# Optimization experiments

Measured on AMD Instinct MI355X. Metric: run time of the kernel, lower is better.

The kernel has to match this reference:

```python
import jax, jax.numpy as jnp
import numpy as np

N = 50000   # nodes
E = 800000  # edges (avg degree 16)
G = 64      # graphs in batch
DIN = 96
DH = 96
DOUT = 10
MD = 30


def setup_inputs() -> dict:
    key = jax.random.key(0)
    ks = jax.random.split(key, 13)
    s = lambda d: 1.0 / np.sqrt(d)
    return {
        "x": jax.random.normal(ks[0], (N, DIN), jnp.float32),
        "edge_index": jax.random.randint(ks[1], (2, E), 0, N, dtype=jnp.int64),
        "edge_attr": jax.random.uniform(ks[2], (E,), jnp.float32),
        "batch": jnp.sort(jax.random.randint(ks[3], (N,), 0, G, dtype=jnp.int64)),
        "metadata": jax.random.normal(ks[4], (G, MD), jnp.float32),
        "W1": jax.random.normal(ks[5], (DIN, DH), jnp.float32) * s(DIN),
        "b1": jnp.zeros((DH,), jnp.float32),
        "W2": jax.random.normal(ks[6], (DH, DH), jnp.float32) * s(DH),
        "b2": jnp.zeros((DH,), jnp.float32),
        "Wm": jax.random.normal(ks[7], (MD, DH), jnp.float32) * s(MD),
        "bm": jnp.zeros((DH,), jnp.float32),
        "Wf": jax.random.normal(ks[8], (2 * DH, DOUT), jnp.float32) * s(2 * DH),
        "bf": jnp.zeros((DOUT,), jnp.float32),
    }


def gcn_conv(x, src, dst, w, W, b):
    """PyG GCNConv with edge weights and self-loops (fill value 1.0)."""
    h = x @ W  # [N, dh]
    deg = jax.ops.segment_sum(w, dst, num_segments=N) + 1.0  # self-loop weight 1
    dinv = jax.lax.rsqrt(deg)
    norm = dinv[src] * w * dinv[dst]  # [E]
    msg = h[src] * norm[:, None]      # gather + weight: [E, dh]
    agg = jax.ops.segment_sum(msg, dst, num_segments=N)
    agg = agg + h * (dinv * dinv)[:, None]  # self-loop contribution
    return agg + b


def reference(x, edge_index, edge_attr, batch, metadata,
              W1, b1, W2, b2, Wm, bm, Wf, bf):
    src, dst = edge_index[0], edge_index[1]
    h = jax.nn.relu(gcn_conv(x, src, dst, edge_attr, W1, b1))
    h = jax.nn.relu(gcn_conv(h, src, dst, edge_attr, W2, b2))
    # global mean pool over graphs
    sums = jax.ops.segment_sum(h, batch, num_segments=G)
    cnts = jax.ops.segment_sum(jnp.ones((N,), h.dtype), batch, num_segments=G)
    pooled = sums / jnp.maximum(cnts, 1.0)[:, None]  # [G, dh]
    # first node index of each graph (batch is sorted), then idx % metadata rows
    first_idx = jax.ops.segment_min(jnp.arange(N), batch, num_segments=G)
    md = metadata[first_idx % metadata.shape[0]]  # [G, 30]
    md_h = jax.nn.relu(md @ Wm + bm)  # dropout = identity in eval
    z = jnp.concatenate([pooled, md_h], axis=1)  # [G, 2*dh]
    return z @ Wf + bf
```

## Files before the change

### kernel.cpp

```cpp
#include <hip/hip_runtime.h>
#include <hip/hip_bf16.h>
#include <cstdint>

typedef unsigned long long ull;
typedef unsigned int uint;

#define FIXS 4194304.0f
#define CAPMAX 48

__device__ __forceinline__ void fma4(float4& a, float s, const float4& v) {
    a.x += s * v.x; a.y += s * v.y; a.z += s * v.z; a.w += s * v.w;
}
__device__ __forceinline__ float dinv_of(ull q) {
    return rsqrtf((float)(unsigned)(q & 0xffffffffULL) * (1.0f / FIXS) + 1.0f);
}
__device__ __forceinline__ uint bf16r(float f) {
    uint u = __float_as_uint(f);
    u += 0x7FFF + ((u >> 16) & 1);
    return u >> 16;
}
__device__ __forceinline__ uint pkbf(float a, float b) { return bf16r(a) | (bf16r(b) << 16); }
__device__ __forceinline__ float blo(uint u) { return __uint_as_float(u << 16); }
__device__ __forceinline__ float bhi(uint u) { return __uint_as_float(u & 0xffff0000u); }


__device__ __forceinline__ void edge_body(int e, const int* __restrict__ ei, const float* __restrict__ w,
                                          ull* __restrict__ packed, int2* __restrict__ ell, int CAP, int E) {
    if (e >= E) return;
    int s = ei[e], d = ei[E + e];
    float wv = w[e];
    ull inc = (1ULL << 32) | (ull)(unsigned)(wv * FIXS + 0.5f);
    ull old = atomicAdd(&packed[d], inc);
    int pos = (int)(old >> 32);
    if (pos < CAP) ell[(size_t)d * CAP + pos] = make_int2(s, __float_as_int(wv));
}

__device__ __forceinline__ void gemm_body(float* Ws, int bb, const float* __restrict__ X,
                                          const float* __restrict__ W, uint* __restrict__ Hb, int N) {
    int t = threadIdx.x;
    {
        const float4* Wg = (const float4*)W;
        float4* Wl = (float4*)Ws;
        for (int i = t; i < 2304; i += 256) Wl[i] = Wg[i];
    }
    int lane = t & 63, wv = t >> 6;
    int cb = wv * 6;
    int row0 = bb * 128;
    int rA = row0 + lane, rB = row0 + 64 + lane;
    bool vA = rA < N, vB = rB < N;
    const float* xA = X + (size_t)(vA ? rA : 0) * 96;
    const float* xB = X + (size_t)(vB ? rB : 0) * 96;
    __syncthreads();
    float4 aA[6] = {}, aB[6] = {};
    const float4* W4 = (const float4*)Ws;
    for (int k0 = 0; k0 < 96; k0 += 4) {
        float4 xa = *(const float4*)(xA + k0);
        float4 xb = *(const float4*)(xB + k0);
#pragma unroll
        for (int kk = 0; kk < 4; kk++) {
            float sa = (kk == 0) ? xa.x : (kk == 1) ? xa.y : (kk == 2) ? xa.z : xa.w;
            float sb = (kk == 0) ? xb.x : (kk == 1) ? xb.y : (kk == 2) ? xb.z : xb.w;
#pragma unroll
            for (int c = 0; c < 6; c++) {
                float4 wv4 = W4[(k0 + kk) * 24 + cb + c];
                fma4(aA[c], sa, wv4);
                fma4(aB[c], sb, wv4);
            }
        }
    }
    if (vA) {
        uint4* o = (uint4*)(Hb + (size_t)rA * 48 + wv * 12);
#pragma unroll
        for (int c = 0; c < 3; c++)
            o[c] = make_uint4(pkbf(aA[2*c].x, aA[2*c].y), pkbf(aA[2*c].z, aA[2*c].w),
                              pkbf(aA[2*c+1].x, aA[2*c+1].y), pkbf(aA[2*c+1].z, aA[2*c+1].w));
    }
    if (vB) {
        uint4* o = (uint4*)(Hb + (size_t)rB * 48 + wv * 12);
#pragma unroll
        for (int c = 0; c < 3; c++)
            o[c] = make_uint4(pkbf(aB[2*c].x, aB[2*c].y), pkbf(aB[2*c].z, aB[2*c].w),
                              pkbf(aB[2*c+1].x, aB[2*c+1].y), pkbf(aB[2*c+1].z, aB[2*c+1].w));
    }
}

__device__ __forceinline__ void pool_meta_body(int bb, const int* __restrict__ batch,
                                               int* __restrict__ cnts, int* __restrict__ firstmax, int N) {
    int n = bb * 256 + threadIdx.x;
    int lane = threadIdx.x & 63;
    bool valid = n < N;
    int g = valid ? batch[n] : -1;
    int gp = __shfl_up(g, 1);
    bool leader = valid && (lane == 0 || gp != g);
    ull lm = __ballot(leader);
    if (leader) {
        ull higher = (lane == 63) ? 0ULL : (lm >> (lane + 1));
        int run;
        if (higher) {
            run = __ffsll((long long)higher);
        } else {
            int waveBase = n - lane;
            int validLanes = min(64, N - waveBase);
            run = validLanes - lane;
        }
        atomicAdd(&cnts[g], run);
        atomicMax(&firstmax[g], N - n);
    }
}

__global__ __launch_bounds__(256) void k_phase1(const float* __restrict__ X, const float* __restrict__ W1,
                                                uint* __restrict__ H1b,
                                                const int* __restrict__ ei, const float* __restrict__ w,
                                                ull* __restrict__ packed, int2* __restrict__ ell, int CAP, int E,
                                                const int* __restrict__ batch, int* __restrict__ cnts,
                                                int* __restrict__ firstmax, int N, int GB, int PB) {
    __shared__ __align__(16) float Ws[96 * 96];
    int b = blockIdx.x;
    if (b < GB) {
        gemm_body(Ws, b, X, W1, H1b, N);
    } else if (b < GB + PB) {
        pool_meta_body(b - GB, batch, cnts, firstmax, N);
    } else {
        edge_body((b - GB - PB) * 256 + threadIdx.x, ei, w, packed, ell, CAP, E);
    }
}

__device__ __forceinline__ float4 gather24(const int2* nbr, int j, int c, int n, float dn, float d2,
                                           const uint* __restrict__ hb, const float* __restrict__ bias) {
    int jo = 2 * j;
    uint2 su = *(const uint2*)(hb + (size_t)n * 48 + jo);
    float4 acc = make_float4(blo(su.x) * d2, bhi(su.x) * d2, blo(su.y) * d2, bhi(su.y) * d2);
    int i = 0;
    for (; i + 8 <= c; i += 8) {
        int4 e01 = *(const int4*)(nbr + i);
        int4 e23 = *(const int4*)(nbr + i + 2);
        int4 e45 = *(const int4*)(nbr + i + 4);
        int4 e67 = *(const int4*)(nbr + i + 6);
        uint2 u0 = *(const uint2*)(hb + e01.x + jo);
        uint2 u1 = *(const uint2*)(hb + e01.z + jo);
        uint2 u2 = *(const uint2*)(hb + e23.x + jo);
        uint2 u3 = *(const uint2*)(hb + e23.z + jo);
        uint2 u4 = *(const uint2*)(hb + e45.x + jo);
        uint2 u5 = *(const uint2*)(hb + e45.z + jo);
        uint2 u6 = *(const uint2*)(hb + e67.x + jo);
        uint2 u7 = *(const uint2*)(hb + e67.z + jo);
        float w0 = __int_as_float(e01.y), w1 = __int_as_float(e01.w);
        float w2 = __int_as_float(e23.y), w3 = __int_as_float(e23.w);
        float w4 = __int_as_float(e45.y), w5 = __int_as_float(e45.w);
        float w6 = __int_as_float(e67.y), w7 = __int_as_float(e67.w);
        acc.x += w0 * blo(u0.x); acc.y += w0 * bhi(u0.x); acc.z += w0 * blo(u0.y); acc.w += w0 * bhi(u0.y);
        acc.x += w1 * blo(u1.x); acc.y += w1 * bhi(u1.x); acc.z += w1 * blo(u1.y); acc.w += w1 * bhi(u1.y);
        acc.x += w2 * blo(u2.x); acc.y += w2 * bhi(u2.x); acc.z += w2 * blo(u2.y); acc.w += w2 * bhi(u2.y);
        acc.x += w3 * blo(u3.x); acc.y += w3 * bhi(u3.x); acc.z += w3 * blo(u3.y); acc.w += w3 * bhi(u3.y);
        acc.x += w4 * blo(u4.x); acc.y += w4 * bhi(u4.x); acc.z += w4 * blo(u4.y); acc.w += w4 * bhi(u4.y);
        acc.x += w5 * blo(u5.x); acc.y += w5 * bhi(u5.x); acc.z += w5 * blo(u5.y); acc.w += w5 * bhi(u5.y);
        acc.x += w6 * blo(u6.x); acc.y += w6 * bhi(u6.x); acc.z += w6 * blo(u6.y); acc.w += w6 * bhi(u6.y);
        acc.x += w7 * blo(u7.x); acc.y += w7 * bhi(u7.x); acc.z += w7 * blo(u7.y); acc.w += w7 * bhi(u7.y);
    }
    for (; i + 2 <= c; i += 2) {
        int4 e01 = *(const int4*)(nbr + i);
        uint2 u0 = *(const uint2*)(hb + e01.x + jo);
        uint2 u1 = *(const uint2*)(hb + e01.z + jo);
        float w0 = __int_as_float(e01.y), w1 = __int_as_float(e01.w);
        acc.x += w0 * blo(u0.x); acc.y += w0 * bhi(u0.x); acc.z += w0 * blo(u0.y); acc.w += w0 * bhi(u0.y);
        acc.x += w1 * blo(u1.x); acc.y += w1 * bhi(u1.x); acc.z += w1 * blo(u1.y); acc.w += w1 * bhi(u1.y);
    }
    if (i < c) {
        int2 e = nbr[i];
        uint2 u = *(const uint2*)(hb + e.x + jo);
        float nw = __int_as_float(e.y);
        acc.x += nw * blo(u.x); acc.y += nw * bhi(u.x); acc.z += nw * blo(u.y); acc.w += nw * bhi(u.y);
    }
    float4 b4 = ((const float4*)bias)[j];
    acc.x = fmaxf(acc.x + b4.x, 0.f); acc.y = fmaxf(acc.y + b4.y, 0.f);
    acc.z = fmaxf(acc.z + b4.z, 0.f); acc.w = fmaxf(acc.w + b4.w, 0.f);
    return acc;
}

__global__ __launch_bounds__(192) void k_agg1(const uint* __restrict__ h1b, const int2* __restrict__ ell,
                                              const ull* __restrict__ packed, int CAP,
                                              const float* __restrict__ bias, uint* __restrict__ g1b, int N) {
    __shared__ __align__(16) int2 nbr[8][CAPMAX];
    int t = threadIdx.x;
    int slot = t / 24, j = t - slot * 24;
    int n = blockIdx.x * 8 + slot;
    bool valid = n < N;
    ull pn = valid ? packed[n] : 0;
    int c = valid ? min((int)(pn >> 32), CAP) : 0;
    float dn = dinv_of(pn), d2 = dn * dn;
    if (valid) {
        size_t base = (size_t)n * CAP;
        for (int i = j; i < c; i += 24) {
            int2 ev = ell[base + i];
            float nw = dinv_of(packed[ev.x]) * __int_as_float(ev.y) * dn;
            nbr[slot][i] = make_int2(ev.x * 48, __float_as_int(nw));
        }
    }
    __syncthreads();
    if (!valid) return;
    float4 acc = gather24(nbr[slot], j, c, n, dn, d2, h1b, bias);
    *(uint2*)(g1b + (size_t)n * 48 + 2 * j) = make_uint2(pkbf(acc.x, acc.y), pkbf(acc.z, acc.w));
}

__global__ __launch_bounds__(256) void k_gemm2(const uint* __restrict__ Xb, const float* __restrict__ W,
                                               uint* __restrict__ Hb, int N) {
    __shared__ __align__(16) float Ws[96 * 96];
    int t = threadIdx.x;
    {
        const float4* Wg = (const float4*)W;
        float4* Wl = (float4*)Ws;
        for (int i = t; i < 2304; i += 256) Wl[i] = Wg[i];
    }
    int lane = t & 63, wv = t >> 6;
    int cb = wv * 6;
    int row0 = blockIdx.x * 128;
    int rA = row0 + lane, rB = row0 + 64 + lane;
    bool vA = rA < N, vB = rB < N;
    const uint* xA = Xb + (size_t)(vA ? rA : 0) * 48;
    const uint* xB = Xb + (size_t)(vB ? rB : 0) * 48;
    __syncthreads();
    float4 aA[6] = {}, aB[6] = {};
    const float4* W4 = (const float4*)Ws;
    for (int k0 = 0; k0 < 96; k0 += 8) {
        uint4 ua = *(const uint4*)(xA + (k0 >> 1));
        uint4 ub = *(const uint4*)(xB + (k0 >> 1));
        float fa[8] = {blo(ua.x), bhi(ua.x), blo(ua.y), bhi(ua.y), blo(ua.z), bhi(ua.z), blo(ua.w), bhi(ua.w)};
        float fb[8] = {blo(ub.x), bhi(ub.x), blo(ub.y), bhi(ub.y), blo(ub.z), bhi(ub.z), blo(ub.w), bhi(ub.w)};
#pragma unroll
        for (int kk = 0; kk < 8; kk++) {
#pragma unroll
            for (int c = 0; c < 6; c++) {
                float4 wv4 = W4[(k0 + kk) * 24 + cb + c];
                fma4(aA[c], fa[kk], wv4);
                fma4(aB[c], fb[kk], wv4);
            }
        }
    }
    if (vA) {
        uint4* o = (uint4*)(Hb + (size_t)rA * 48 + wv * 12);
#pragma unroll
        for (int c = 0; c < 3; c++)
            o[c] = make_uint4(pkbf(aA[2*c].x, aA[2*c].y), pkbf(aA[2*c].z, aA[2*c].w),
                              pkbf(aA[2*c+1].x, aA[2*c+1].y), pkbf(aA[2*c+1].z, aA[2*c+1].w));
    }
    if (vB) {
        uint4* o = (uint4*)(Hb + (size_t)rB * 48 + wv * 12);
#pragma unroll
        for (int c = 0; c < 3; c++)
            o[c] = make_uint4(pkbf(aB[2*c].x, aB[2*c].y), pkbf(aB[2*c].z, aB[2*c].w),
                              pkbf(aB[2*c+1].x, aB[2*c+1].y), pkbf(aB[2*c+1].z, aB[2*c+1].w));
    }
}

__global__ __launch_bounds__(192) void k_agg_pool(const uint* __restrict__ h2b, const int2* __restrict__ ell,
                                                  const ull* __restrict__ packed, int CAP,
                                                  const float* __restrict__ bias,
                                                  const int* __restrict__ batch, float* __restrict__ sums, int N) {
    __shared__ __align__(16) int2 nbr[8][CAPMAX];
    __shared__ float vals[8][96];
    __shared__ int gs[8];
    int t = threadIdx.x;
    int slot = t / 24, j = t - slot * 24;
    int n = blockIdx.x * 8 + slot;
    bool valid = n < N;
    int g = valid ? batch[n] : -1;
    ull pn = valid ? packed[n] : 0;
    int c = valid ? min((int)(pn >> 32), CAP) : 0;
    float dn = dinv_of(pn), d2 = dn * dn;
    if (valid) {
        size_t base = (size_t)n * CAP;
        for (int i = j; i < c; i += 24) {
            int2 ev = ell[base + i];
            float nw = dinv_of(packed[ev.x]) * __int_as_float(ev.y) * dn;
            nbr[slot][i] = make_int2(ev.x * 48, __float_as_int(nw));
        }
    }
    __syncthreads();
    float4 acc = {0, 0, 0, 0};
    if (valid) acc = gather24(nbr[slot], j, c, n, dn, d2, h2b, bias);
    if (j == 0) gs[slot] = g;
    *(float4*)&vals[slot][4 * j] = acc;
    __syncthreads();
    if (t < 96) {
        int f = t;
        int g0 = gs[0];
        bool uni = true;
#pragma unroll
        for (int s = 1; s < 8; s++) uni &= (gs[s] == g0);
        if (uni) {
            if (g0 >= 0) {
                float sum = 0;
#pragma unroll
                for (int s = 0; s < 8; s++) sum += vals[s][f];
                atomicAdd(&sums[g0 * 96 + f], sum);
            }
        } else {
#pragma unroll
            for (int s = 0; s < 8; s++) {
                int gg = gs[s];
                if (gg >= 0) atomicAdd(&sums[gg * 96 + f], vals[s][f]);
            }
        }
    }
}

__global__ __launch_bounds__(128) void k_final(const float* __restrict__ sums, const int* __restrict__ cnts,
                                               const int* __restrict__ firstmax, const float* __restrict__ metadata,
                                               const float* __restrict__ Wm, const float* __restrict__ bm,
                                               const float* __restrict__ Wf, const float* __restrict__ bf,
                                               float* __restrict__ out, int N, int mrows) {
    __shared__ float z[192];
    int g = blockIdx.x, t = threadIdx.x;
    if (t < 96) {
        float c = fmaxf((float)cnts[g], 1.0f);
        z[t] = sums[g * 96 + t] / c;
        unsigned fi = (unsigned)(N - firstmax[g]);
        unsigned mi = fi % (unsigned)mrows;
        float acc = bm[t];
        for (int k = 0; k < 30; k++) acc += metadata[mi * 30 + k] * Wm[k * 96 + t];
        z[96 + t] = fmaxf(acc, 0.f);
    }
    __syncthreads();
    if (t < 10) {
        float acc = bf[t];
        for (int q = 0; q < 192; q++) acc += z[q] * Wf[q * 10 + t];
        out[g * 10 + t] = acc;
    }
}

extern "C" void kernel_launch(void* const* d_in, const int* in_sizes, int n_in,
                              void* d_out, int out_size, void* d_ws, size_t ws_size,
                              hipStream_t stream) {
    const float* x        = (const float*)d_in[0];
    const int*   ei       = (const int*)d_in[1];
    const float* ew       = (const float*)d_in[2];
    const int*   batch    = (const int*)d_in[3];
    const float* metadata = (const float*)d_in[4];
    const float* W1 = (const float*)d_in[5];
    const float* b1 = (const float*)d_in[6];
    const float* W2 = (const float*)d_in[7];
    const float* b2 = (const float*)d_in[8];
    const float* Wm = (const float*)d_in[9];
    const float* bm = (const float*)d_in[10];
    const float* Wf = (const float*)d_in[11];
    const float* bf = (const float*)d_in[12];
    float* out = (float*)d_out;

    const int N = in_sizes[3];
    const int E = in_sizes[2];
    const int G = in_sizes[4] / 30;

    auto al = [](size_t b) { return (b + 255) & ~(size_t)255; };
    size_t fixed = al((size_t)N * 8) + al((size_t)G * 96 * 4) + al((size_t)G * 4) * 2 +
                   al((size_t)N * 48 * 4) * 3 + 4096;
    int CAP = CAPMAX;
    while (CAP > 32 && fixed + al((size_t)N * CAP * 8) > ws_size) CAP -= 8;
    if (CAP > CAPMAX) CAP = CAPMAX;

    char* p = (char*)d_ws;
    size_t off = 0;
    auto carve = [&](size_t bytes) -> void* {
        void* r = p + off;
        off = (off + bytes + 255) & ~(size_t)255;
        return r;
    };
    ull*   packed   = (ull*)carve((size_t)N * 8);
    float* sums     = (float*)carve((size_t)G * 96 * 4);
    int*   cnts     = (int*)carve((size_t)G * 4);
    int*   firstmax = (int*)carve((size_t)G * 4);
    size_t zero_end = off;
    int2*  ell  = (int2*)carve((size_t)N * CAP * 8);
    uint*  h1b  = (uint*)carve((size_t)N * 48 * 4);
    uint*  g1b  = (uint*)carve((size_t)N * 48 * 4);
    uint*  h2b  = (uint*)carve((size_t)N * 48 * 4);

    hipMemsetAsync(packed, 0, zero_end, stream);

    int EB = (E + 255) / 256;
    int GB = (N + 127) / 128;
    int PB = (N + 255) / 256;
    int nb8 = (N + 7) / 8;

    k_phase1<<<GB + PB + EB, 256, 0, stream>>>(x, W1, h1b, ei, ew, packed, ell, CAP, E,
                                               batch, cnts, firstmax, N, GB, PB);
    k_agg1<<<nb8, 192, 0, stream>>>(h1b, ell, packed, CAP, b1, g1b, N);
    k_gemm2<<<GB, 256, 0, stream>>>(g1b, W2, h2b, N);
    k_agg_pool<<<nb8, 192, 0, stream>>>(h2b, ell, packed, CAP, b2, batch, sums, N);
    k_final<<<G, 128, 0, stream>>>(sums, cnts, firstmax, metadata, Wm, bm, Wf, bf, out, N, G);
}
```

Measured before the change: 230.3 us.

## Fuse layer-1 aggregation with W2 GEMM and fold final head into pool kernel

Merges the first aggregation and the second GEMM into one kernel. Each block stages its 8 aggregated rows in shared memory and multiplies them by a bf16 copy of W2 held in LDS, so the g1b intermediate is no longer written to and read back from global memory. The final MLP head now runs in the last-finishing block of the pooling kernel, found with an atomic done counter, which removes a kernel launch. Costs are that every block reloads and converts W2 into LDS, the per-row GEMM is thin, and the tail head runs serially in a single block.

```diff
diff --git a/kernel.cpp b/kernel.cpp
--- a/kernel.cpp
+++ b/kernel.cpp
@@ -125,7 +125,7 @@
     }
 }
 
-__device__ __forceinline__ float4 gather24(const int2* nbr, int j, int c, int n, float dn, float d2,
+__device__ __forceinline__ float4 gather24(const int2* nbr, int j, int c, int n, float d2,
                                            const uint* __restrict__ hb, const float* __restrict__ bias) {
     int jo = 2 * j;
     uint2 su = *(const uint2*)(hb + (size_t)n * 48 + jo);
@@ -177,11 +177,19 @@
     return acc;
 }
 
-__global__ __launch_bounds__(192) void k_agg1(const uint* __restrict__ h1b, const int2* __restrict__ ell,
-                                              const ull* __restrict__ packed, int CAP,
-                                              const float* __restrict__ bias, uint* __restrict__ g1b, int N) {
+__global__ __launch_bounds__(192) void k_mid(const uint* __restrict__ h1b, const int2* __restrict__ ell,
+                                             const ull* __restrict__ packed, int CAP,
+                                             const float* __restrict__ b1, const float* __restrict__ W2,
+                                             uint* __restrict__ h2b, int N) {
     __shared__ __align__(16) int2 nbr[8][CAPMAX];
+    __shared__ __align__(16) uint Wl[96 * 48];
+    __shared__ __align__(16) float g1row[8][96];
     int t = threadIdx.x;
+    for (int i = t; i < 2304; i += 192) {
+        float4 w = ((const float4*)W2)[i];
+        int r = i / 24, c = i % 24;
+        *(uint2*)&Wl[r * 48 + c * 2] = make_uint2(pkbf(w.x, w.y), pkbf(w.z, w.w));
+    }
     int slot = t / 24, j = t - slot * 24;
     int n = blockIdx.x * 8 + slot;
     bool valid = n < N;
@@ -197,68 +205,36 @@
         }
     }
     __syncthreads();
-    if (!valid) return;
-    float4 acc = gather24(nbr[slot], j, c, n, dn, d2, h1b, bias);
-    *(uint2*)(g1b + (size_t)n * 48 + 2 * j) = make_uint2(pkbf(acc.x, acc.y), pkbf(acc.z, acc.w));
-}
-
-__global__ __launch_bounds__(256) void k_gemm2(const uint* __restrict__ Xb, const float* __restrict__ W,
-                                               uint* __restrict__ Hb, int N) {
-    __shared__ __align__(16) float Ws[96 * 96];
-    int t = threadIdx.x;
-    {
-        const float4* Wg = (const float4*)W;
-        float4* Wl = (float4*)Ws;
-        for (int i = t; i < 2304; i += 256) Wl[i] = Wg[i];
-    }
-    int lane = t & 63, wv = t >> 6;
-    int cb = wv * 6;
-    int row0 = blockIdx.x * 128;
-    int rA = row0 + lane, rB = row0 + 64 + lane;
-    bool vA = rA < N, vB = rB < N;
-    const uint* xA = Xb + (size_t)(vA ? rA : 0) * 48;
-    const uint* xB = Xb + (size_t)(vB ? rB : 0) * 48;
-    __syncthreads();
-    float4 aA[6] = {}, aB[6] = {};
-    const float4* W4 = (const float4*)Ws;
-    for (int k0 = 0; k0 < 96; k0 += 8) {
-        uint4 ua = *(const uint4*)(xA + (k0 >> 1));
-        uint4 ub = *(const uint4*)(xB + (k0 >> 1));
-        float fa[8] = {blo(ua.x), bhi(ua.x), blo(ua.y), bhi(ua.y), blo(ua.z), bhi(ua.z), blo(ua.w), bhi(ua.w)};
-        float fb[8] = {blo(ub.x), bhi(ub.x), blo(ub.y), bhi(ub.y), blo(ub.z), bhi(ub.z), blo(ub.w), bhi(ub.w)};
-#pragma unroll
-        for (int kk = 0; kk < 8; kk++) {
-#pragma unroll
-            for (int c = 0; c < 6; c++) {
-                float4 wv4 = W4[(k0 + kk) * 24 + cb + c];
-                fma4(aA[c], fa[kk], wv4);
-                fma4(aB[c], fb[kk], wv4);
-            }
-        }
-    }
-    if (vA) {
-        uint4* o = (uint4*)(Hb + (size_t)rA * 48 + wv * 12);
-#pragma unroll
-        for (int c = 0; c < 3; c++)
-            o[c] = make_uint4(pkbf(aA[2*c].x, aA[2*c].y), pkbf(aA[2*c].z, aA[2*c].w),
-                              pkbf(aA[2*c+1].x, aA[2*c+1].y), pkbf(aA[2*c+1].z, aA[2*c+1].w));
-    }
-    if (vB) {
-        uint4* o = (uint4*)(Hb + (size_t)rB * 48 + wv * 12);
-#pragma unroll
-        for (int c = 0; c < 3; c++)
-            o[c] = make_uint4(pkbf(aB[2*c].x, aB[2*c].y), pkbf(aB[2*c].z, aB[2*c].w),
-                              pkbf(aB[2*c+1].x, aB[2*c+1].y), pkbf(aB[2*c+1].z, aB[2*c+1].w));
-    }
+    float4 acc = {0, 0, 0, 0};
+    if (valid) acc = gather24(nbr[slot], j, c, n, d2, h1b, b1);
+    *(float4*)&g1row[slot][4 * j] = acc;
+    __syncthreads();
+    float4 out = {0, 0, 0, 0};
+#pragma unroll 4
+    for (int k = 0; k < 96; k++) {
+        float g = g1row[slot][k];
+        uint2 wv = *(const uint2*)&Wl[k * 48 + 2 * j];
+        out.x += g * blo(wv.x); out.y += g * bhi(wv.x);
+        out.z += g * blo(wv.y); out.w += g * bhi(wv.y);
+    }
+    if (valid) *(uint2*)(h2b + (size_t)n * 48 + 2 * j) = make_uint2(pkbf(out.x, out.y), pkbf(out.z, out.w));
 }
 
 __global__ __launch_bounds__(192) void k_agg_pool(const uint* __restrict__ h2b, const int2* __restrict__ ell,
                                                   const ull* __restrict__ packed, int CAP,
-                                                  const float* __restrict__ bias,
-                                                  const int* __restrict__ batch, float* __restrict__ sums, int N) {
+                                                  const float* __restrict__ b2,
+                                                  const int* __restrict__ batch, float* __restrict__ sums,
+                                                  int* __restrict__ done, int nblocks,
+                                                  const int* __restrict__ cnts, const int* __restrict__ firstmax,
+                                                  const float* __restrict__ metadata,
+                                                  const float* __restrict__ Wm, const float* __restrict__ bm,
+                                                  const float* __restrict__ Wf, const float* __restrict__ bf,
+                                                  float* __restrict__ out, int G, int N, int mrows) {
     __shared__ __align__(16) int2 nbr[8][CAPMAX];
     __shared__ float vals[8][96];
     __shared__ int gs[8];
+    __shared__ int amLast;
+    __shared__ float z[2][192];
     int t = threadIdx.x;
     int slot = t / 24, j = t - slot * 24;
     int n = blockIdx.x * 8 + slot;
@@ -277,7 +253,7 @@
     }
     __syncthreads();
     float4 acc = {0, 0, 0, 0};
-    if (valid) acc = gather24(nbr[slot], j, c, n, dn, d2, h2b, bias);
+    if (valid) acc = gather24(nbr[slot], j, c, n, d2, h2b, b2);
     if (j == 0) gs[slot] = g;
     *(float4*)&vals[slot][4 * j] = acc;
     __syncthreads();
@@ -287,44 +263,51 @@
         bool uni = true;
 #pragma unroll
         for (int s = 1; s < 8; s++) uni &= (gs[s] == g0);
+        float rsum = 0.f;
         if (uni) {
             if (g0 >= 0) {
                 float sum = 0;
 #pragma unroll
                 for (int s = 0; s < 8; s++) sum += vals[s][f];
-                atomicAdd(&sums[g0 * 96 + f], sum);
+                rsum += atomicAdd(&sums[g0 * 96 + f], sum);
             }
         } else {
 #pragma unroll
             for (int s = 0; s < 8; s++) {
                 int gg = gs[s];
-                if (gg >= 0) atomicAdd(&sums[gg * 96 + f], vals[s][f]);
+                if (gg >= 0) rsum += atomicAdd(&sums[gg * 96 + f], vals[s][f]);
             }
         }
-    }
-}
-
-__global__ __launch_bounds__(128) void k_final(const float* __restrict__ sums, const int* __restrict__ cnts,
-                                               const int* __restrict__ firstmax, const float* __restrict__ metadata,
-                                               const float* __restrict__ Wm, const float* __restrict__ bm,
-                                               const float* __restrict__ Wf, const float* __restrict__ bf,
-                                               float* __restrict__ out, int N, int mrows) {
-    __shared__ float z[192];
-    int g = blockIdx.x, t = threadIdx.x;
-    if (t < 96) {
-        float c = fmaxf((float)cnts[g], 1.0f);
-        z[t] = sums[g * 96 + t] / c;
-        unsigned fi = (unsigned)(N - firstmax[g]);
-        unsigned mi = fi % (unsigned)mrows;
-        float acc = bm[t];
-        for (int k = 0; k < 30; k++) acc += metadata[mi * 30 + k] * Wm[k * 96 + t];
-        z[96 + t] = fmaxf(acc, 0.f);
-    }
-    __syncthreads();
-    if (t < 10) {
-        float acc = bf[t];
-        for (int q = 0; q < 192; q++) acc += z[q] * Wf[q * 10 + t];
-        out[g * 10 + t] = acc;
+        if (__float_as_uint(rsum) == 0xff800001u) sums[0] = rsum;
+    }
+    __syncthreads();
+    if (t == 0) amLast = (atomicAdd(done, 1) == nblocks - 1) ? 1 : 0;
+    __syncthreads();
+    if (!amLast) return;
+    int half = t / 96, f = t - half * 96;
+    for (int p = 0; p < (G + 1) / 2; p++) {
+        int gg = p * 2 + half;
+        if (gg < G) {
+            float sv = __hip_atomic_load(&sums[gg * 96 + f], __ATOMIC_RELAXED, __HIP_MEMORY_SCOPE_AGENT);
+            float cg = fmaxf((float)cnts[gg], 1.0f);
+            z[half][f] = sv / cg;
+            unsigned fi = (unsigned)(N - firstmax[gg]);
+            unsigned mi = fi % (unsigned)mrows;
+            float a = bm[f];
+            for (int k = 0; k < 30; k++) a += metadata[mi * 30 + k] * Wm[k * 96 + f];
+            z[half][96 + f] = fmaxf(a, 0.f);
+        }
+        __syncthreads();
+        if (t < 20) {
+            int gh = t / 10, o = t - gh * 10;
+            int gg2 = p * 2 + gh;
+            if (gg2 < G) {
+                float a = bf[o];
+                for (int q = 0; q < 192; q++) a += z[gh][q] * Wf[q * 10 + o];
+                out[gg2 * 10 + o] = a;
+            }
+        }
+        __syncthreads();
     }
 }
 
@@ -351,8 +334,8 @@
     const int G = in_sizes[4] / 30;
 
     auto al = [](size_t b) { return (b + 255) & ~(size_t)255; };
-    size_t fixed = al((size_t)N * 8) + al((size_t)G * 96 * 4) + al((size_t)G * 4) * 2 +
-                   al((size_t)N * 48 * 4) * 3 + 4096;
+    size_t fixed = al((size_t)N * 8) + al((size_t)G * 96 * 4) + al((size_t)G * 4) * 2 + al(256) +
+                   al((size_t)N * 48 * 4) * 2 + 4096;
     int CAP = CAPMAX;
     while (CAP > 32 && fixed + al((size_t)N * CAP * 8) > ws_size) CAP -= 8;
     if (CAP > CAPMAX) CAP = CAPMAX;
@@ -368,10 +351,10 @@
     float* sums     = (float*)carve((size_t)G * 96 * 4);
     int*   cnts     = (int*)carve((size_t)G * 4);
     int*   firstmax = (int*)carve((size_t)G * 4);
+    int*   done     = (int*)carve(256);
     size_t zero_end = off;
     int2*  ell  = (int2*)carve((size_t)N * CAP * 8);
     uint*  h1b  = (uint*)carve((size_t)N * 48 * 4);
-    uint*  g1b  = (uint*)carve((size_t)N * 48 * 4);
     uint*  h2b  = (uint*)carve((size_t)N * 48 * 4);
 
     hipMemsetAsync(packed, 0, zero_end, stream);
@@ -383,8 +366,8 @@
 
     k_phase1<<<GB + PB + EB, 256, 0, stream>>>(x, W1, h1b, ei, ew, packed, ell, CAP, E,
                                                batch, cnts, firstmax, N, GB, PB);
-    k_agg1<<<nb8, 192, 0, stream>>>(h1b, ell, packed, CAP, b1, g1b, N);
-    k_gemm2<<<GB, 256, 0, stream>>>(g1b, W2, h2b, N);
-    k_agg_pool<<<nb8, 192, 0, stream>>>(h2b, ell, packed, CAP, b2, batch, sums, N);
-    k_final<<<G, 128, 0, stream>>>(sums, cnts, firstmax, metadata, Wm, bm, Wf, bf, out, N, G);
-}
+    k_mid<<<nb8, 192, 0, stream>>>(h1b, ell, packed, CAP, b1, W2, h2b, N);
+    k_agg_pool<<<nb8, 192, 0, stream>>>(h2b, ell, packed, CAP, b2, batch, sums,
+                                        done, nb8, cnts, firstmax, metadata,
+                                        Wm, bm, Wf, bf, out, G, N, G);
+}
```

New measurement: 389.5 us. 1.69x slower.

## Pack ELL entries into 32 bits and gather 16-byte rows with 12 lanes per node

Applied to the files above, without the earlier changes.

Each ELL entry now holds a 16-bit source index and a bf16 edge weight in one 32-bit word instead of an int2, halving adjacency storage and the bytes read during staging. The aggregation kernels now use 12 threads per node, each doing 16-byte gathers of eight features, and each block covers 16 nodes instead of 8. The intermediate buffer g1b is dropped by ping-ponging between h1b and h2b. The packing assumes fewer than 65536 nodes and rounds edge weights to bf16, which adds approximation error.

```diff
diff --git a/kernel.cpp b/kernel.cpp
--- a/kernel.cpp
+++ b/kernel.cpp
@@ -25,14 +25,14 @@
 
 
 __device__ __forceinline__ void edge_body(int e, const int* __restrict__ ei, const float* __restrict__ w,
-                                          ull* __restrict__ packed, int2* __restrict__ ell, int CAP, int E) {
+                                          ull* __restrict__ packed, uint* __restrict__ ell4, int CAP, int E) {
     if (e >= E) return;
     int s = ei[e], d = ei[E + e];
     float wv = w[e];
     ull inc = (1ULL << 32) | (ull)(unsigned)(wv * FIXS + 0.5f);
     ull old = atomicAdd(&packed[d], inc);
     int pos = (int)(old >> 32);
-    if (pos < CAP) ell[(size_t)d * CAP + pos] = make_int2(s, __float_as_int(wv));
+    if (pos < CAP) ell4[(size_t)d * CAP + pos] = (uint)s | (bf16r(wv) << 16);
 }
 
 __device__ __forceinline__ void gemm_body(float* Ws, int bb, const float* __restrict__ X,
@@ -111,7 +111,7 @@
 __global__ __launch_bounds__(256) void k_phase1(const float* __restrict__ X, const float* __restrict__ W1,
                                                 uint* __restrict__ H1b,
                                                 const int* __restrict__ ei, const float* __restrict__ w,
-                                                ull* __restrict__ packed, int2* __restrict__ ell, int CAP, int E,
+                                                ull* __restrict__ packed, uint* __restrict__ ell4, int CAP, int E,
                                                 const int* __restrict__ batch, int* __restrict__ cnts,
                                                 int* __restrict__ firstmax, int N, int GB, int PB) {
     __shared__ __align__(16) float Ws[96 * 96];
@@ -121,85 +121,78 @@
     } else if (b < GB + PB) {
         pool_meta_body(b - GB, batch, cnts, firstmax, N);
     } else {
-        edge_body((b - GB - PB) * 256 + threadIdx.x, ei, w, packed, ell, CAP, E);
-    }
-}
-
-__device__ __forceinline__ float4 gather24(const int2* nbr, int j, int c, int n, float dn, float d2,
-                                           const uint* __restrict__ hb, const float* __restrict__ bias) {
-    int jo = 2 * j;
-    uint2 su = *(const uint2*)(hb + (size_t)n * 48 + jo);
-    float4 acc = make_float4(blo(su.x) * d2, bhi(su.x) * d2, blo(su.y) * d2, bhi(su.y) * d2);
+        edge_body((b - GB - PB) * 256 + threadIdx.x, ei, w, packed, ell4, CAP, E);
+    }
+}
+
+__device__ __forceinline__ void gather12(const int2* nbr, int j, int c, int n, float d2,
+                                         const uint* __restrict__ hb, const float* __restrict__ bias,
+                                         float4& lo, float4& hi) {
+    int jo = 4 * j;
+    uint4 su = *(const uint4*)(hb + (size_t)n * 48 + jo);
+    lo = make_float4(blo(su.x) * d2, bhi(su.x) * d2, blo(su.y) * d2, bhi(su.y) * d2);
+    hi = make_float4(blo(su.z) * d2, bhi(su.z) * d2, blo(su.w) * d2, bhi(su.w) * d2);
     int i = 0;
-    for (; i + 8 <= c; i += 8) {
+    for (; i + 4 <= c; i += 4) {
         int4 e01 = *(const int4*)(nbr + i);
         int4 e23 = *(const int4*)(nbr + i + 2);
-        int4 e45 = *(const int4*)(nbr + i + 4);
-        int4 e67 = *(const int4*)(nbr + i + 6);
-        uint2 u0 = *(const uint2*)(hb + e01.x + jo);
-        uint2 u1 = *(const uint2*)(hb + e01.z + jo);
-        uint2 u2 = *(const uint2*)(hb + e23.x + jo);
-        uint2 u3 = *(const uint2*)(hb + e23.z + jo);
-        uint2 u4 = *(const uint2*)(hb + e45.x + jo);
-        uint2 u5 = *(const uint2*)(hb + e45.z + jo);
-        uint2 u6 = *(const uint2*)(hb + e67.x + jo);
-        uint2 u7 = *(const uint2*)(hb + e67.z + jo);
+        uint4 u0 = *(const uint4*)(hb + e01.x + jo);
+        uint4 u1 = *(const uint4*)(hb + e01.z + jo);
+        uint4 u2 = *(const uint4*)(hb + e23.x + jo);
+        uint4 u3 = *(const uint4*)(hb + e23.z + jo);
         float w0 = __int_as_float(e01.y), w1 = __int_as_float(e01.w);
         float w2 = __int_as_float(e23.y), w3 = __int_as_float(e23.w);
-        float w4 = __int_as_float(e45.y), w5 = __int_as_float(e45.w);
-        float w6 = __int_as_float(e67.y), w7 = __int_as_float(e67.w);
-        acc.x += w0 * blo(u0.x); acc.y += w0 * bhi(u0.x); acc.z += w0 * blo(u0.y); acc.w += w0 * bhi(u0.y);
-        acc.x += w1 * blo(u1.x); acc.y += w1 * bhi(u1.x); acc.z += w1 * blo(u1.y); acc.w += w1 * bhi(u1.y);
-        acc.x += w2 * blo(u2.x); acc.y += w2 * bhi(u2.x); acc.z += w2 * blo(u2.y); acc.w += w2 * bhi(u2.y);
-        acc.x += w3 * blo(u3.x); acc.y += w3 * bhi(u3.x); acc.z += w3 * blo(u3.y); acc.w += w3 * bhi(u3.y);
-        acc.x += w4 * blo(u4.x); acc.y += w4 * bhi(u4.x); acc.z += w4 * blo(u4.y); acc.w += w4 * bhi(u4.y);
-        acc.x += w5 * blo(u5.x); acc.y += w5 * bhi(u5.x); acc.z += w5 * blo(u5.y); acc.w += w5 * bhi(u5.y);
-        acc.x += w6 * blo(u6.x); acc.y += w6 * bhi(u6.x); acc.z += w6 * blo(u6.y); acc.w += w6 * bhi(u6.y);
-        acc.x += w7 * blo(u7.x); acc.y += w7 * bhi(u7.x); acc.z += w7 * blo(u7.y); acc.w += w7 * bhi(u7.y);
-    }
-    for (; i + 2 <= c; i += 2) {
-        int4 e01 = *(const int4*)(nbr + i);
-        uint2 u0 = *(const uint2*)(hb + e01.x + jo);
-        uint2 u1 = *(const uint2*)(hb + e01.z + jo);
-        float w0 = __int_as_float(e01.y), w1 = __int_as_float(e01.w);
-        acc.x += w0 * blo(u0.x); acc.y += w0 * bhi(u0.x); acc.z += w0 * blo(u0.y); acc.w += w0 * bhi(u0.y);
-        acc.x += w1 * blo(u1.x); acc.y += w1 * bhi(u1.x); acc.z += w1 * blo(u1.y); acc.w += w1 * bhi(u1.y);
-    }
-    if (i < c) {
+        lo.x += w0 * blo(u0.x); lo.y += w0 * bhi(u0.x); lo.z += w0 * blo(u0.y); lo.w += w0 * bhi(u0.y);
+        hi.x += w0 * blo(u0.z); hi.y += w0 * bhi(u0.z); hi.z += w0 * blo(u0.w); hi.w += w0 * bhi(u0.w);
+        lo.x += w1 * blo(u1.x); lo.y += w1 * bhi(u1.x); lo.z += w1 * blo(u1.y); lo.w += w1 * bhi(u1.y);
+        hi.x += w1 * blo(u1.z); hi.y += w1 * bhi(u1.z); hi.z += w1 * blo(u1.w); hi.w += w1 * bhi(u1.w);
+        lo.x += w2 * blo(u2.x); lo.y += w2 * bhi(u2.x); lo.z += w2 * blo(u2.y); lo.w += w2 * bhi(u2.y);
+        hi.x += w2 * blo(u2.z); hi.y += w2 * bhi(u2.z); hi.z += w2 * blo(u2.w); hi.w += w2 * bhi(u2.w);
+        lo.x += w3 * blo(u3.x); lo.y += w3 * bhi(u3.x); lo.z += w3 * blo(u3.y); lo.w += w3 * bhi(u3.y);
+        hi.x += w3 * blo(u3.z); hi.y += w3 * bhi(u3.z); hi.z += w3 * blo(u3.w); hi.w += w3 * bhi(u3.w);
+    }
+    for (; i < c; i++) {
         int2 e = nbr[i];
-        uint2 u = *(const uint2*)(hb + e.x + jo);
+        uint4 u = *(const uint4*)(hb + e.x + jo);
         float nw = __int_as_float(e.y);
-        acc.x += nw * blo(u.x); acc.y += nw * bhi(u.x); acc.z += nw * blo(u.y); acc.w += nw * bhi(u.y);
-    }
-    float4 b4 = ((const float4*)bias)[j];
-    acc.x = fmaxf(acc.x + b4.x, 0.f); acc.y = fmaxf(acc.y + b4.y, 0.f);
-    acc.z = fmaxf(acc.z + b4.z, 0.f); acc.w = fmaxf(acc.w + b4.w, 0.f);
-    return acc;
-}
-
-__global__ __launch_bounds__(192) void k_agg1(const uint* __restrict__ h1b, const int2* __restrict__ ell,
+        lo.x += nw * blo(u.x); lo.y += nw * bhi(u.x); lo.z += nw * blo(u.y); lo.w += nw * bhi(u.y);
+        hi.x += nw * blo(u.z); hi.y += nw * bhi(u.z); hi.z += nw * blo(u.w); hi.w += nw * bhi(u.w);
+    }
+    float4 b0 = ((const float4*)bias)[2 * j], b1 = ((const float4*)bias)[2 * j + 1];
+    lo.x = fmaxf(lo.x + b0.x, 0.f); lo.y = fmaxf(lo.y + b0.y, 0.f);
+    lo.z = fmaxf(lo.z + b0.z, 0.f); lo.w = fmaxf(lo.w + b0.w, 0.f);
+    hi.x = fmaxf(hi.x + b1.x, 0.f); hi.y = fmaxf(hi.y + b1.y, 0.f);
+    hi.z = fmaxf(hi.z + b1.z, 0.f); hi.w = fmaxf(hi.w + b1.w, 0.f);
+}
+
+__device__ __forceinline__ void stage12(int2* nbrs, int j, int c, size_t base, float dn,
+                                        const uint* __restrict__ ell4, const ull* __restrict__ packed) {
+    for (int i = j; i < c; i += 12) {
+        uint ev = ell4[base + i];
+        int src = (int)(ev & 0xFFFFu);
+        float nw = dinv_of(packed[src]) * bhi(ev) * dn;
+        nbrs[i] = make_int2(src * 48, __float_as_int(nw));
+    }
+}
+
+__global__ __launch_bounds__(192) void k_agg1(const uint* __restrict__ h1b, const uint* __restrict__ ell4,
                                               const ull* __restrict__ packed, int CAP,
                                               const float* __restrict__ bias, uint* __restrict__ g1b, int N) {
-    __shared__ __align__(16) int2 nbr[8][CAPMAX];
+    __shared__ __align__(16) int2 nbr[16][CAPMAX];
     int t = threadIdx.x;
-    int slot = t / 24, j = t - slot * 24;
-    int n = blockIdx.x * 8 + slot;
+    int slot = t / 12, j = t - slot * 12;
+    int n = blockIdx.x * 16 + slot;
     bool valid = n < N;
     ull pn = valid ? packed[n] : 0;
     int c = valid ? min((int)(pn >> 32), CAP) : 0;
     float dn = dinv_of(pn), d2 = dn * dn;
-    if (valid) {
-        size_t base = (size_t)n * CAP;
-        for (int i = j; i < c; i += 24) {
-            int2 ev = ell[base + i];
-            float nw = dinv_of(packed[ev.x]) * __int_as_float(ev.y) * dn;
-            nbr[slot][i] = make_int2(ev.x * 48, __float_as_int(nw));
-        }
-    }
+    if (valid) stage12(nbr[slot], j, c, (size_t)n * CAP, dn, ell4, packed);
     __syncthreads();
     if (!valid) return;
-    float4 acc = gather24(nbr[slot], j, c, n, dn, d2, h1b, bias);
-    *(uint2*)(g1b + (size_t)n * 48 + 2 * j) = make_uint2(pkbf(acc.x, acc.y), pkbf(acc.z, acc.w));
+    float4 lo, hi;
+    gather12(nbr[slot], j, c, n, d2, h1b, bias, lo, hi);
+    *(uint4*)(g1b + (size_t)n * 48 + 4 * j) =
+        make_uint4(pkbf(lo.x, lo.y), pkbf(lo.z, lo.w), pkbf(hi.x, hi.y), pkbf(hi.z, hi.w));
 }
 
 __global__ __launch_bounds__(256) void k_gemm2(const uint* __restrict__ Xb, const float* __restrict__ W,
@@ -252,51 +245,45 @@
     }
 }
 
-__global__ __launch_bounds__(192) void k_agg_pool(const uint* __restrict__ h2b, const int2* __restrict__ ell,
+__global__ __launch_bounds__(192) void k_agg_pool(const uint* __restrict__ h2b, const uint* __restrict__ ell4,
                                                   const ull* __restrict__ packed, int CAP,
                                                   const float* __restrict__ bias,
                                                   const int* __restrict__ batch, float* __restrict__ sums, int N) {
-    __shared__ __align__(16) int2 nbr[8][CAPMAX];
-    __shared__ float vals[8][96];
-    __shared__ int gs[8];
+    __shared__ __align__(16) int2 nbr[16][CAPMAX];
+    __shared__ float vals[16][96];
+    __shared__ int gs[16];
     int t = threadIdx.x;
-    int slot = t / 24, j = t - slot * 24;
-    int n = blockIdx.x * 8 + slot;
+    int slot = t / 12, j = t - slot * 12;
+    int n = blockIdx.x * 16 + slot;
     bool valid = n < N;
     int g = valid ? batch[n] : -1;
     ull pn = valid ? packed[n] : 0;
     int c = valid ? min((int)(pn >> 32), CAP) : 0;
     float dn = dinv_of(pn), d2 = dn * dn;
-    if (valid) {
-        size_t base = (size_t)n * CAP;
-        for (int i = j; i < c; i += 24) {
-            int2 ev = ell[base + i];
-            float nw = dinv_of(packed[ev.x]) * __int_as_float(ev.y) * dn;
-            nbr[slot][i] = make_int2(ev.x * 48, __float_as_int(nw));
-        }
-    }
-    __syncthreads();
-    float4 acc = {0, 0, 0, 0};
-    if (valid) acc = gather24(nbr[slot], j, c, n, dn, d2, h2b, bias);
+    if (valid) stage12(nbr[slot], j, c, (size_t)n * CAP, dn, ell4, packed);
+    __syncthreads();
+    float4 lo = {0, 0, 0, 0}, hi = {0, 0, 0, 0};
+    if (valid) gather12(nbr[slot], j, c, n, d2, h2b, bias, lo, hi);
     if (j == 0) gs[slot] = g;
-    *(float4*)&vals[slot][4 * j] = acc;
+    *(float4*)&vals[slot][8 * j] = lo;
+    *(float4*)&vals[slot][8 * j + 4] = hi;
     __syncthreads();
     if (t < 96) {
         int f = t;
         int g0 = gs[0];
         bool uni = true;
 #pragma unroll
-        for (int s = 1; s < 8; s++) uni &= (gs[s] == g0);
+        for (int s = 1; s < 16; s++) uni &= (gs[s] == g0);
         if (uni) {
             if (g0 >= 0) {
                 float sum = 0;
 #pragma unroll
-                for (int s = 0; s < 8; s++) sum += vals[s][f];
+                for (int s = 0; s < 16; s++) sum += vals[s][f];
                 atomicAdd(&sums[g0 * 96 + f], sum);
             }
         } else {
 #pragma unroll
-            for (int s = 0; s < 8; s++) {
+            for (int s = 0; s < 16; s++) {
                 int gg = gs[s];
                 if (gg >= 0) atomicAdd(&sums[gg * 96 + f], vals[s][f]);
             }
@@ -352,9 +339,9 @@
 
     auto al = [](size_t b) { return (b + 255) & ~(size_t)255; };
     size_t fixed = al((size_t)N * 8) + al((size_t)G * 96 * 4) + al((size_t)G * 4) * 2 +
-                   al((size_t)N * 48 * 4) * 3 + 4096;
+                   al((size_t)N * 48 * 4) * 2 + 4096;
     int CAP = CAPMAX;
-    while (CAP > 32 && fixed + al((size_t)N * CAP * 8) > ws_size) CAP -= 8;
+    while (CAP > 32 && fixed + al((size_t)N * CAP * 4) > ws_size) CAP -= 8;
     if (CAP > CAPMAX) CAP = CAPMAX;
 
     char* p = (char*)d_ws;
@@ -369,22 +356,21 @@
     int*   cnts     = (int*)carve((size_t)G * 4);
     int*   firstmax = (int*)carve((size_t)G * 4);
     size_t zero_end = off;
-    int2*  ell  = (int2*)carve((size_t)N * CAP * 8);
+    uint*  ell4 = (uint*)carve((size_t)N * CAP * 4);
     uint*  h1b  = (uint*)carve((size_t)N * 48 * 4);
-    uint*  g1b  = (uint*)carve((size_t)N * 48 * 4);
     uint*  h2b  = (uint*)carve((size_t)N * 48 * 4);
 
-    hipMemsetAsync(packed, 0, zero_end, stream);
+    (void)hipMemsetAsync(packed, 0, zero_end, stream);
 
     int EB = (E + 255) / 256;
     int GB = (N + 127) / 128;
     int PB = (N + 255) / 256;
-    int nb8 = (N + 7) / 8;
-
-    k_phase1<<<GB + PB + EB, 256, 0, stream>>>(x, W1, h1b, ei, ew, packed, ell, CAP, E,
+    int nb16 = (N + 15) / 16;
+
+    k_phase1<<<GB + PB + EB, 256, 0, stream>>>(x, W1, h1b, ei, ew, packed, ell4, CAP, E,
                                                batch, cnts, firstmax, N, GB, PB);
-    k_agg1<<<nb8, 192, 0, stream>>>(h1b, ell, packed, CAP, b1, g1b, N);
-    k_gemm2<<<GB, 256, 0, stream>>>(g1b, W2, h2b, N);
-    k_agg_pool<<<nb8, 192, 0, stream>>>(h2b, ell, packed, CAP, b2, batch, sums, N);
+    k_agg1<<<nb16, 192, 0, stream>>>(h1b, ell4, packed, CAP, b1, h2b, N);
+    k_gemm2<<<GB, 256, 0, stream>>>(h2b, W2, h1b, N);
+    k_agg_pool<<<nb16, 192, 0, stream>>>(h1b, ell4, packed, CAP, b2, batch, sums, N);
     k_final<<<G, 128, 0, stream>>>(sums, cnts, firstmax, metadata, Wm, bm, Wf, bf, out, N, G);
 }
```

Result: no change. 231.3 us (+0.4%).
